# Kernel tuning notes

Hardware: AMD Instinct MI355X
Metric: run time of the kernel (lower is better)

Reference implementation:

```python
import jax, jax.numpy as jnp
import numpy as np

H = 10   # GRU hidden size
L = 10   # num layers
E = 400  # embedding dim
V = 100000
T, B = 84, 96


def gru_layer(x, w_ih, w_hh, b_ih, b_hh, reverse):
    # x: (T, B, in_dim); w_ih: (3H, in_dim); w_hh: (3H, H)
    xp = jnp.einsum('tbi,gi->tbg', x, w_ih) + b_ih  # (T, B, 3H)
    if reverse:
        xp = xp[::-1]

    def step(h, xt):
        gh = h @ w_hh.T + b_hh
        xr, xz, xn = jnp.split(xt, 3, axis=-1)
        hr, hz, hn = jnp.split(gh, 3, axis=-1)
        r = jax.nn.sigmoid(xr + hr)
        z = jax.nn.sigmoid(xz + hz)
        n = jnp.tanh(xn + r * hn)
        h_new = (1.0 - z) * n + z * h
        return h_new, h_new

    h0 = jnp.zeros((x.shape[1], H), x.dtype)
    _, ys = jax.lax.scan(step, h0, xp)
    if reverse:
        ys = ys[::-1]
    return ys  # (T, B, H)


def setup_inputs():
    key = jax.random.key(0)
    ks = jax.random.split(key, 12)
    s = 0.05
    return {
        'x': jax.random.randint(ks[0], (T, B), 0, V),
        'emb': jax.random.normal(ks[1], (V, E), jnp.float32) * 0.1,
        'w_ih0': jax.random.normal(ks[2], (2, 3 * H, E), jnp.float32) * s,
        'w_hh0': jax.random.normal(ks[3], (2, 3 * H, H), jnp.float32) * s,
        'b_ih0': jax.random.normal(ks[4], (2, 3 * H), jnp.float32) * s,
        'b_hh0': jax.random.normal(ks[5], (2, 3 * H), jnp.float32) * s,
        'w_ih': jax.random.normal(ks[6], (L - 1, 2, 3 * H, 2 * H), jnp.float32) * s,
        'w_hh': jax.random.normal(ks[7], (L - 1, 2, 3 * H, H), jnp.float32) * s,
        'b_ih': jax.random.normal(ks[8], (L - 1, 2, 3 * H), jnp.float32) * s,
        'b_hh': jax.random.normal(ks[9], (L - 1, 2, 3 * H), jnp.float32) * s,
        'lin_w': jax.random.normal(ks[10], (19, 336), jnp.float32) * s,
        'lin_b': jax.random.normal(ks[11], (19,), jnp.float32) * s,
    }


def reference(x, emb, w_ih0, w_hh0, b_ih0, b_hh0, w_ih, w_hh, b_ih, b_hh, lin_w, lin_b):
    out = emb[x]  # (T, B, 400)
    for l in range(L):
        if l == 0:
            wi, wh, bi, bh = w_ih0, w_hh0, b_ih0, b_hh0
        else:
            wi, wh, bi, bh = w_ih[l - 1], w_hh[l - 1], b_ih[l - 1], b_hh[l - 1]
        fwd = gru_layer(out, wi[0], wh[0], bi[0], bh[0], False)
        bwd = gru_layer(out, wi[1], wh[1], bi[1], bh[1], True)
        out = jnp.concatenate([fwd, bwd], axis=-1)  # (T, B, 20)
        # dropout p=0.2 between layers is disabled (eval-mode reference)
    # AvgPool2d(3)/MaxPool2d(3) on 3D input pool over (batch, feature) dims
    trimmed = out[:, : (B // 3) * 3, :18].reshape(T, B // 3, 3, 6, 3)
    avg = trimmed.mean(axis=(2, 4))  # (T, B//3, 6)
    mx = trimmed.max(axis=(2, 4))    # (T, B//3, 6)
    cat = jnp.concatenate([avg, mx], axis=2)  # (T, B//3, 12)
    flat = cat.reshape(-1, 336)  # (96, 336)
    # dropout p=0.2 disabled (eval-mode reference)
    return jax.nn.sigmoid(flat @ lin_w.T + lin_b)
```

## Files before the change

kernel.cpp:

```cpp
#include <hip/hip_runtime.h>
#include <math.h>

#define TT 84
#define BB 96
#define GB 6
#define NG 16
#define NTOK (TT*BB)
#define RW4 6

#define S_RZ (-1.4426950408889634f)
#define S_N  (-2.8853900817779268f)

__device__ __forceinline__ float frcp(float x)  { return __builtin_amdgcn_rcpf(x); }
__device__ __forceinline__ float fexp2(float x) { return __builtin_amdgcn_exp2f(x); }

__global__ __launch_bounds__(256) void proj0_kernel(
    const int* __restrict__ x, const float* __restrict__ emb,
    const float* __restrict__ wih0, const float* __restrict__ bih0,
    float* __restrict__ xp, unsigned int* __restrict__ bar)
{
    if (blockIdx.x == 0 && threadIdx.x == 0) bar[0] = 0u;
    __shared__ float4 xrow[32][100];
    const int tok0 = blockIdx.x * 32;
    for (int u = threadIdx.x; u < 32*100; u += 256) {
        int tk = u / 100, i4 = u % 100;
        int row = x[tok0 + tk];
        xrow[tk][i4] = ((const float4*)emb)[row*100 + i4];
    }
    __syncthreads();
    const int g64 = threadIdx.x & 63;
    const int q   = threadIdx.x >> 6;
    if (g64 >= 60) return;
    const int dir = g64 / 30, gg = g64 % 30;
    const float sc = (gg < 20) ? S_RZ : S_N;
    const float bias = bih0[dir*30 + gg];
    float acc[8];
    #pragma unroll
    for (int c = 0; c < 8; ++c) acc[c] = bias;
    const float4* w4 = ((const float4*)wih0) + (dir*30 + gg)*100;
    for (int i4 = 0; i4 < 100; ++i4) {
        float4 w = w4[i4];
        #pragma unroll
        for (int c = 0; c < 8; ++c) {
            float4 xv = xrow[q*8 + c][i4];
            acc[c] += w.x*xv.x + w.y*xv.y + w.z*xv.z + w.w*xv.w;
        }
    }
    #pragma unroll
    for (int c = 0; c < 8; ++c) {
        int tok = tok0 + q*8 + c;
        int t = tok / BB, b = tok % BB;
        xp[((size_t)((dir*TT + t)*BB + b))*30 + gg] = acc[c]*sc;
    }
}

__device__ __forceinline__ float gru_cell(
    float xr, float xz, float xn,
    float4 ha, float4 hb, float4 hc,
    const float* wr, const float* wz, const float* wn,
    float bhr, float bhz, float bhn, float& hown)
{
    float hr0 = fmaf(wr[0], ha.x, bhr), hr1 = wr[1]*ha.y;
    float hz0 = fmaf(wz[0], ha.x, bhz), hz1 = wz[1]*ha.y;
    float hn0 = fmaf(wn[0], ha.x, bhn), hn1 = wn[1]*ha.y;
    hr0 = fmaf(wr[2], ha.z, hr0); hr1 = fmaf(wr[3], ha.w, hr1);
    hz0 = fmaf(wz[2], ha.z, hz0); hz1 = fmaf(wz[3], ha.w, hz1);
    hn0 = fmaf(wn[2], ha.z, hn0); hn1 = fmaf(wn[3], ha.w, hn1);
    hr0 = fmaf(wr[4], hb.x, hr0); hr1 = fmaf(wr[5], hb.y, hr1);
    hz0 = fmaf(wz[4], hb.x, hz0); hz1 = fmaf(wz[5], hb.y, hz1);
    hn0 = fmaf(wn[4], hb.x, hn0); hn1 = fmaf(wn[5], hb.y, hn1);
    hr0 = fmaf(wr[6], hb.z, hr0); hr1 = fmaf(wr[7], hb.w, hr1);
    hz0 = fmaf(wz[6], hb.z, hz0); hz1 = fmaf(wz[7], hb.w, hz1);
    hn0 = fmaf(wn[6], hb.z, hn0); hn1 = fmaf(wn[7], hb.w, hn1);
    hr0 = fmaf(wr[8], hc.x, hr0); hr1 = fmaf(wr[9], hc.y, hr1);
    hz0 = fmaf(wz[8], hc.x, hz0); hz1 = fmaf(wz[9], hc.y, hz1);
    hn0 = fmaf(wn[8], hc.x, hn0); hn1 = fmaf(wn[9], hc.y, hn1);
    float r = frcp(1.f + fexp2(xr + hr0 + hr1));
    float z = frcp(1.f + fexp2(xz + hz0 + hz1));
    float an = fmaf(r, hn0 + hn1, xn);
    float n  = fmaf(2.f, frcp(1.f + fexp2(an)), -1.f);
    float hnew = n + z*(hown - n);
    hown = hnew;
    return hnew;
}

__device__ __forceinline__ void proj20(
    const float4* A, const float* wpr, const float* wpz, const float* wpn,
    float bir, float biz, float bin, float& xr, float& xz, float& xn)
{
    float a[24];
    #pragma unroll
    for (int q = 0; q < 6; ++q) {
        a[4*q]=A[q].x; a[4*q+1]=A[q].y; a[4*q+2]=A[q].z; a[4*q+3]=A[q].w;
    }
    xr = bir; xz = biz; xn = bin;
    #pragma unroll
    for (int c = 0; c < 20; ++c) {
        float av = a[c + (c >= 10 ? 2 : 0)];
        xr = fmaf(wpr[c], av, xr); xz = fmaf(wpz[c], av, xz); xn = fmaf(wpn[c], av, xn);
    }
}

template<bool LAST>
__device__ __forceinline__ void gru_mid(
    const float* __restrict__ wi, const float* __restrict__ bi,
    const float* __restrict__ wh, const float* __restrict__ bh,
    const float4* in4, float4* out4, float* __restrict__ actG,
    int bl, int j, bool act_ln, int b, int dir, int dt, int t0)
{
    float wpr[20], wpz[20], wpn[20];
    {
        const float4* p0 = (const float4*)(wi + j*20);
        const float4* p1 = (const float4*)(wi + (10+j)*20);
        const float4* p2 = (const float4*)(wi + (20+j)*20);
        #pragma unroll
        for (int q = 0; q < 5; ++q) {
            float4 a = p0[q]; wpr[4*q]=a.x*S_RZ; wpr[4*q+1]=a.y*S_RZ; wpr[4*q+2]=a.z*S_RZ; wpr[4*q+3]=a.w*S_RZ;
            float4 c = p1[q]; wpz[4*q]=c.x*S_RZ; wpz[4*q+1]=c.y*S_RZ; wpz[4*q+2]=c.z*S_RZ; wpz[4*q+3]=c.w*S_RZ;
            float4 d = p2[q]; wpn[4*q]=d.x*S_N;  wpn[4*q+1]=d.y*S_N;  wpn[4*q+2]=d.z*S_N;  wpn[4*q+3]=d.w*S_N;
        }
    }
    const float bir = bi[j]*S_RZ, biz = bi[10+j]*S_RZ, bin = bi[20+j]*S_N;
    float wr[10], wz[10], wn[10];
    {
        const float2* p0 = (const float2*)(wh + j*10);
        const float2* p1 = (const float2*)(wh + (10+j)*10);
        const float2* p2 = (const float2*)(wh + (20+j)*10);
        #pragma unroll
        for (int q = 0; q < 5; ++q) {
            float2 a = p0[q]; wr[2*q]=a.x*S_RZ; wr[2*q+1]=a.y*S_RZ;
            float2 c = p1[q]; wz[2*q]=c.x*S_RZ; wz[2*q+1]=c.y*S_RZ;
            float2 d = p2[q]; wn[2*q]=d.x*S_N;  wn[2*q+1]=d.y*S_N;
        }
    }
    const float bhr = bh[j]*S_RZ, bhz = bh[10+j]*S_RZ, bhn = bh[20+j]*S_N;

    float4 ha = {0,0,0,0}, hb = {0,0,0,0}, hc = {0,0,0,0};
    float hown = 0.f;
    float4 A[6], B[6];
    float xr_c, xz_c, xn_c, xr_n, xz_n, xn_n;
    int t = t0;
    {
        const float4* p0 = &in4[(t0*GB + bl)*RW4];
        #pragma unroll
        for (int q = 0; q < 6; ++q) B[q] = p0[q];
        const float4* p1 = &in4[((t0 + dt)*GB + bl)*RW4];
        #pragma unroll
        for (int q = 0; q < 6; ++q) A[q] = p1[q];
        proj20(B, wpr, wpz, wpn, bir, biz, bin, xr_c, xz_c, xn_c);
    }

    #pragma unroll 1
    for (int s = 0; s < TT; s += 2) {
        {
            float hnew = gru_cell(xr_c, xz_c, xn_c, ha, hb, hc, wr, wz, wn, bhr, bhz, bhn, hown);
            ((float*)&out4[(t*GB + bl)*RW4])[dir*12 + j] = hnew;
            const float4* hr = &out4[(t*GB + bl)*RW4 + dir*3];
            ha = hr[0]; hb = hr[1]; hc = hr[2];
            __builtin_amdgcn_sched_barrier(0);
            if (LAST && act_ln) actG[(size_t)(t*BB + b)*20 + dir*10 + j] = hnew;
            int tl = t + 2*dt; tl = tl < 0 ? 0 : (tl > TT-1 ? TT-1 : tl);
            const float4* pl = &in4[(tl*GB + bl)*RW4];
            #pragma unroll
            for (int q = 0; q < 6; ++q) B[q] = pl[q];
            proj20(A, wpr, wpz, wpn, bir, biz, bin, xr_n, xz_n, xn_n);
            t += dt;
        }
        {
            float hnew = gru_cell(xr_n, xz_n, xn_n, ha, hb, hc, wr, wz, wn, bhr, bhz, bhn, hown);
            ((float*)&out4[(t*GB + bl)*RW4])[dir*12 + j] = hnew;
            const float4* hr = &out4[(t*GB + bl)*RW4 + dir*3];
            ha = hr[0]; hb = hr[1]; hc = hr[2];
            __builtin_amdgcn_sched_barrier(0);
            if (LAST && act_ln) actG[(size_t)(t*BB + b)*20 + dir*10 + j] = hnew;
            int tl = t + 2*dt; tl = tl < 0 ? 0 : (tl > TT-1 ? TT-1 : tl);
            const float4* pl = &in4[(tl*GB + bl)*RW4];
            #pragma unroll
            for (int q = 0; q < 6; ++q) A[q] = pl[q];
            proj20(B, wpr, wpz, wpn, bir, biz, bin, xr_c, xz_c, xn_c);
            t += dt;
        }
    }
}

__global__ __launch_bounds__(128, 1) void mega_kernel(
    const float* __restrict__ xp0,
    const float* __restrict__ whh0, const float* __restrict__ bhh0,
    const float* __restrict__ wih,  const float* __restrict__ bih,
    const float* __restrict__ whh,  const float* __restrict__ bhh,
    const float* __restrict__ lin_w, const float* __restrict__ lin_b,
    float* __restrict__ actG, unsigned int* __restrict__ bar,
    float* __restrict__ out)
{
    __shared__ float4 actA4[TT*GB*RW4];
    __shared__ float4 actB4[TT*GB*RW4];

    const int tid  = threadIdx.x;
    const int dir  = tid >> 6;
    const int lane = tid & 63;
    int bl = lane / 10; if (bl > 5) bl = 5;
    int j  = lane - bl*10; if (j > 9) j = 9;
    const bool act_ln = (lane < 60);
    const int grp = blockIdx.x;
    const int b   = grp*GB + bl;
    const int dt  = dir ? -1 : 1;
    const int t0  = dir ? TT-1 : 0;

    {
        float wr[10], wz[10], wn[10];
        const float* wh = whh0 + dir*300;
        {
            const float2* p0 = (const float2*)(wh + j*10);
            const float2* p1 = (const float2*)(wh + (10+j)*10);
            const float2* p2 = (const float2*)(wh + (20+j)*10);
            #pragma unroll
            for (int q = 0; q < 5; ++q) {
                float2 a = p0[q]; wr[2*q]=a.x*S_RZ; wr[2*q+1]=a.y*S_RZ;
                float2 c = p1[q]; wz[2*q]=c.x*S_RZ; wz[2*q+1]=c.y*S_RZ;
                float2 d = p2[q]; wn[2*q]=d.x*S_N;  wn[2*q+1]=d.y*S_N;
            }
        }
        const float bhr = bhh0[dir*30 + j]*S_RZ;
        const float bhz = bhh0[dir*30 + 10 + j]*S_RZ;
        const float bhn = bhh0[dir*30 + 20 + j]*S_N;

        float4 ha = {0,0,0,0}, hb = {0,0,0,0}, hc = {0,0,0,0};
        float hown = 0.f;
        int t = t0;
        const float* xb = xp0 + (size_t)dir*TT*BB*30;

        float xr_c = xb[(size_t)(t*BB + b)*30 + j];
        float xz_c = xb[(size_t)(t*BB + b)*30 + 10 + j];
        float xn_c = xb[(size_t)(t*BB + b)*30 + 20 + j];

        #pragma unroll 1
        for (int s = 0; s < TT; ++s) {
            float hnew = gru_cell(xr_c, xz_c, xn_c, ha, hb, hc, wr, wz, wn, bhr, bhz, bhn, hown);
            ((float*)&actA4[(t*GB + bl)*RW4])[dir*12 + j] = hnew;
            const float4* hr = &actA4[(t*GB + bl)*RW4 + dir*3];
            ha = hr[0]; hb = hr[1]; hc = hr[2];
            __builtin_amdgcn_sched_barrier(0);
            int tn = (s == TT-1) ? t : t + dt;
            xr_c = xb[(size_t)(tn*BB + b)*30 + j];
            xz_c = xb[(size_t)(tn*BB + b)*30 + 10 + j];
            xn_c = xb[(size_t)(tn*BB + b)*30 + 20 + j];
            t = tn;
        }
    }
    __syncthreads();

    #pragma unroll 1
    for (int lp = 0; lp < 4; ++lp) {
        int l = 1 + lp*2;
        gru_mid<false>(wih + (size_t)((l-1)*2 + dir)*600, bih + (size_t)((l-1)*2 + dir)*30,
                       whh + (size_t)((l-1)*2 + dir)*300, bhh + (size_t)((l-1)*2 + dir)*30,
                       actA4, actB4, actG, bl, j, act_ln, b, dir, dt, t0);
        __syncthreads();
        l = 2 + lp*2;
        gru_mid<false>(wih + (size_t)((l-1)*2 + dir)*600, bih + (size_t)((l-1)*2 + dir)*30,
                       whh + (size_t)((l-1)*2 + dir)*300, bhh + (size_t)((l-1)*2 + dir)*30,
                       actB4, actA4, actG, bl, j, act_ln, b, dir, dt, t0);
        __syncthreads();
    }
    gru_mid<true>(wih + (size_t)(8*2 + dir)*600, bih + (size_t)(8*2 + dir)*30,
                  whh + (size_t)(8*2 + dir)*300, bhh + (size_t)(8*2 + dir)*30,
                  actA4, actB4, actG, bl, j, act_ln, b, dir, dt, t0);

    __threadfence();
    __syncthreads();
    if (tid == 0) {
        __hip_atomic_fetch_add(bar, 1u, __ATOMIC_ACQ_REL, __HIP_MEMORY_SCOPE_AGENT);
        while (__hip_atomic_load(bar, __ATOMIC_ACQUIRE, __HIP_MEMORY_SCOPE_AGENT) < (unsigned)NG)
            __builtin_amdgcn_s_sleep(1);
    }
    __syncthreads();
    __threadfence();

    float* feat = (float*)actA4;
    for (int u = tid; u < GB*336; u += 128) {
        int q = u / 336, v = u % 336;
        int r = grp*GB + q;
        int qq = v / 12, f = v % 12;
        int pair = r*28 + qq;
        int t = pair / 32, bb = pair % 32;
        int jj = (f < 6) ? f : f - 6;
        float acc = (f < 6) ? 0.f : -1e30f;
        #pragma unroll
        for (int i = 0; i < 3; ++i) {
            #pragma unroll
            for (int kk = 0; kk < 3; ++kk) {
                float vv = actG[(size_t)(t*BB + bb*3 + i)*20 + jj*3 + kk];
                if (f < 6) acc += vv; else acc = fmaxf(acc, vv);
            }
        }
        feat[u] = (f < 6) ? acc*(1.f/9.f) : acc;
    }
    __syncthreads();
    if (tid < GB*19) {
        int q = tid / 19, o = tid % 19;
        int r = grp*GB + q;
        float acc = lin_b[o];
        const float* wrow = lin_w + o*336;
        const float* frow = feat + q*336;
        for (int v = 0; v < 336; ++v) acc = fmaf(frow[v], wrow[v], acc);
        out[r*19 + o] = frcp(1.f + __expf(-acc));
    }
}

extern "C" void kernel_launch(void* const* d_in, const int* in_sizes, int n_in,
                              void* d_out, int out_size, void* d_ws, size_t ws_size,
                              hipStream_t stream)
{
    const int*   x     = (const int*)  d_in[0];
    const float* emb   = (const float*)d_in[1];
    const float* wih0  = (const float*)d_in[2];
    const float* whh0  = (const float*)d_in[3];
    const float* bih0  = (const float*)d_in[4];
    const float* bhh0  = (const float*)d_in[5];
    const float* wih   = (const float*)d_in[6];
    const float* whh   = (const float*)d_in[7];
    const float* bih   = (const float*)d_in[8];
    const float* bhh   = (const float*)d_in[9];
    const float* lin_w = (const float*)d_in[10];
    const float* lin_b = (const float*)d_in[11];
    float* out = (float*)d_out;

    float* xp0  = (float*)d_ws;
    float* actG = xp0 + (size_t)2*NTOK*30;
    unsigned int* bar = (unsigned int*)(actG + (size_t)NTOK*20);

    proj0_kernel<<<252, 256, 0, stream>>>(x, emb, wih0, bih0, xp0, bar);
    mega_kernel<<<NG, 128, 0, stream>>>(xp0, whh0, bhh0, wih, bih, whh, bhh,
                                        lin_w, lin_b, actG, bar, out);
}
```

Measured before the change: 485.9 us.

## Split GRU layers into producer projection waves and consumer recurrence waves

Each block now runs 256 threads. Two waves compute the input projection for a layer and publish each timestep into shared memory, signalling progress through per-layer flags. The other two waves run the serial recurrence and spin on those flags, so the 20-wide projection leaves the recurrent critical path. Inter-layer activations move from shared memory to global buffers, and the hidden-state exchange uses a small shared buffer. The cost is flag polling, global-memory activation traffic, and the second activation buffer aliasing the layer-0 projection workspace, which other blocks may still be reading.

```diff
diff --git a/kernel.cpp b/kernel.cpp
--- a/kernel.cpp
+++ b/kernel.cpp
@@ -5,8 +5,9 @@
 #define BB 96
 #define GB 6
 #define NG 16
+#define NL 10
 #define NTOK (TT*BB)
-#define RW4 6
+#define XPS 37
 
 #define S_RZ (-1.4426950408889634f)
 #define S_N  (-2.8853900817779268f)
@@ -56,7 +57,7 @@
 
 __device__ __forceinline__ float gru_cell(
     float xr, float xz, float xn,
-    float4 ha, float4 hb, float4 hc,
+    float4 ha, float4 hb, float2 hc,
     const float* wr, const float* wz, const float* wn,
     float bhr, float bhz, float bhn, float& hown)
 {
@@ -84,187 +85,168 @@
     return hnew;
 }
 
-__device__ __forceinline__ void proj20(
-    const float4* A, const float* wpr, const float* wpz, const float* wpn,
-    float bir, float biz, float bin, float& xr, float& xz, float& xn)
-{
-    float a[24];
-    #pragma unroll
-    for (int q = 0; q < 6; ++q) {
-        a[4*q]=A[q].x; a[4*q+1]=A[q].y; a[4*q+2]=A[q].z; a[4*q+3]=A[q].w;
-    }
-    xr = bir; xz = biz; xn = bin;
-    #pragma unroll
-    for (int c = 0; c < 20; ++c) {
-        float av = a[c + (c >= 10 ? 2 : 0)];
-        xr = fmaf(wpr[c], av, xr); xz = fmaf(wpz[c], av, xz); xn = fmaf(wpn[c], av, xn);
-    }
-}
-
-template<bool LAST>
-__device__ __forceinline__ void gru_mid(
-    const float* __restrict__ wi, const float* __restrict__ bi,
-    const float* __restrict__ wh, const float* __restrict__ bh,
-    const float4* in4, float4* out4, float* __restrict__ actG,
-    int bl, int j, bool act_ln, int b, int dir, int dt, int t0)
-{
-    float wpr[20], wpz[20], wpn[20];
-    {
-        const float4* p0 = (const float4*)(wi + j*20);
-        const float4* p1 = (const float4*)(wi + (10+j)*20);
-        const float4* p2 = (const float4*)(wi + (20+j)*20);
-        #pragma unroll
-        for (int q = 0; q < 5; ++q) {
-            float4 a = p0[q]; wpr[4*q]=a.x*S_RZ; wpr[4*q+1]=a.y*S_RZ; wpr[4*q+2]=a.z*S_RZ; wpr[4*q+3]=a.w*S_RZ;
-            float4 c = p1[q]; wpz[4*q]=c.x*S_RZ; wpz[4*q+1]=c.y*S_RZ; wpz[4*q+2]=c.z*S_RZ; wpz[4*q+3]=c.w*S_RZ;
-            float4 d = p2[q]; wpn[4*q]=d.x*S_N;  wpn[4*q+1]=d.y*S_N;  wpn[4*q+2]=d.z*S_N;  wpn[4*q+3]=d.w*S_N;
-        }
-    }
-    const float bir = bi[j]*S_RZ, biz = bi[10+j]*S_RZ, bin = bi[20+j]*S_N;
-    float wr[10], wz[10], wn[10];
-    {
-        const float2* p0 = (const float2*)(wh + j*10);
-        const float2* p1 = (const float2*)(wh + (10+j)*10);
-        const float2* p2 = (const float2*)(wh + (20+j)*10);
-        #pragma unroll
-        for (int q = 0; q < 5; ++q) {
-            float2 a = p0[q]; wr[2*q]=a.x*S_RZ; wr[2*q+1]=a.y*S_RZ;
-            float2 c = p1[q]; wz[2*q]=c.x*S_RZ; wz[2*q+1]=c.y*S_RZ;
-            float2 d = p2[q]; wn[2*q]=d.x*S_N;  wn[2*q+1]=d.y*S_N;
-        }
-    }
-    const float bhr = bh[j]*S_RZ, bhz = bh[10+j]*S_RZ, bhn = bh[20+j]*S_N;
-
-    float4 ha = {0,0,0,0}, hb = {0,0,0,0}, hc = {0,0,0,0};
-    float hown = 0.f;
-    float4 A[6], B[6];
-    float xr_c, xz_c, xn_c, xr_n, xz_n, xn_n;
-    int t = t0;
-    {
-        const float4* p0 = &in4[(t0*GB + bl)*RW4];
-        #pragma unroll
-        for (int q = 0; q < 6; ++q) B[q] = p0[q];
-        const float4* p1 = &in4[((t0 + dt)*GB + bl)*RW4];
-        #pragma unroll
-        for (int q = 0; q < 6; ++q) A[q] = p1[q];
-        proj20(B, wpr, wpz, wpn, bir, biz, bin, xr_c, xz_c, xn_c);
-    }
-
-    #pragma unroll 1
-    for (int s = 0; s < TT; s += 2) {
-        {
-            float hnew = gru_cell(xr_c, xz_c, xn_c, ha, hb, hc, wr, wz, wn, bhr, bhz, bhn, hown);
-            ((float*)&out4[(t*GB + bl)*RW4])[dir*12 + j] = hnew;
-            const float4* hr = &out4[(t*GB + bl)*RW4 + dir*3];
-            ha = hr[0]; hb = hr[1]; hc = hr[2];
-            __builtin_amdgcn_sched_barrier(0);
-            if (LAST && act_ln) actG[(size_t)(t*BB + b)*20 + dir*10 + j] = hnew;
-            int tl = t + 2*dt; tl = tl < 0 ? 0 : (tl > TT-1 ? TT-1 : tl);
-            const float4* pl = &in4[(tl*GB + bl)*RW4];
-            #pragma unroll
-            for (int q = 0; q < 6; ++q) B[q] = pl[q];
-            proj20(A, wpr, wpz, wpn, bir, biz, bin, xr_n, xz_n, xn_n);
-            t += dt;
-        }
-        {
-            float hnew = gru_cell(xr_n, xz_n, xn_n, ha, hb, hc, wr, wz, wn, bhr, bhz, bhn, hown);
-            ((float*)&out4[(t*GB + bl)*RW4])[dir*12 + j] = hnew;
-            const float4* hr = &out4[(t*GB + bl)*RW4 + dir*3];
-            ha = hr[0]; hb = hr[1]; hc = hr[2];
-            __builtin_amdgcn_sched_barrier(0);
-            if (LAST && act_ln) actG[(size_t)(t*BB + b)*20 + dir*10 + j] = hnew;
-            int tl = t + 2*dt; tl = tl < 0 ? 0 : (tl > TT-1 ? TT-1 : tl);
-            const float4* pl = &in4[(tl*GB + bl)*RW4];
-            #pragma unroll
-            for (int q = 0; q < 6; ++q) A[q] = pl[q];
-            proj20(B, wpr, wpz, wpn, bir, biz, bin, xr_c, xz_c, xn_c);
-            t += dt;
-        }
-    }
-}
-
-__global__ __launch_bounds__(128, 1) void mega_kernel(
+__device__ __forceinline__ void waitflag(int* f, int needed)
+{
+    int fv = __hip_atomic_load(f, __ATOMIC_ACQUIRE, __HIP_MEMORY_SCOPE_WORKGROUP);
+    while (fv < needed)
+        fv = __hip_atomic_load(f, __ATOMIC_ACQUIRE, __HIP_MEMORY_SCOPE_WORKGROUP);
+}
+
+__global__ __launch_bounds__(256, 1) void mega_kernel(
     const float* __restrict__ xp0,
     const float* __restrict__ whh0, const float* __restrict__ bhh0,
     const float* __restrict__ wih,  const float* __restrict__ bih,
     const float* __restrict__ whh,  const float* __restrict__ bhh,
     const float* __restrict__ lin_w, const float* __restrict__ lin_b,
-    float* __restrict__ actG, unsigned int* __restrict__ bar,
-    float* __restrict__ out)
-{
-    __shared__ float4 actA4[TT*GB*RW4];
-    __shared__ float4 actB4[TT*GB*RW4];
+    float* __restrict__ actA, float* __restrict__ actB,
+    unsigned int* __restrict__ bar, float* __restrict__ out)
+{
+    __shared__ float xpS[2*TT*GB*XPS];
+    __shared__ float hbuf[2][GB][12];
+    __shared__ int   flagsS[NL][2];
 
     const int tid  = threadIdx.x;
-    const int dir  = tid >> 6;
+    const int wave = tid >> 6;
     const int lane = tid & 63;
     int bl = lane / 10; if (bl > 5) bl = 5;
     int j  = lane - bl*10; if (j > 9) j = 9;
     const bool act_ln = (lane < 60);
     const int grp = blockIdx.x;
     const int b   = grp*GB + bl;
+
+    if (tid < NL*2) ((int*)flagsS)[tid] = 0;
+    __syncthreads();
+
+    const int dir = wave & 1;
     const int dt  = dir ? -1 : 1;
     const int t0  = dir ? TT-1 : 0;
 
-    {
-        float wr[10], wz[10], wn[10];
-        const float* wh = whh0 + dir*300;
-        {
-            const float2* p0 = (const float2*)(wh + j*10);
-            const float2* p1 = (const float2*)(wh + (10+j)*10);
-            const float2* p2 = (const float2*)(wh + (20+j)*10);
-            #pragma unroll
-            for (int q = 0; q < 5; ++q) {
-                float2 a = p0[q]; wr[2*q]=a.x*S_RZ; wr[2*q+1]=a.y*S_RZ;
-                float2 c = p1[q]; wz[2*q]=c.x*S_RZ; wz[2*q+1]=c.y*S_RZ;
-                float2 d = p2[q]; wn[2*q]=d.x*S_N;  wn[2*q+1]=d.y*S_N;
+    #pragma unroll 1
+    for (int l = 0; l < NL; ++l) {
+        if (wave < 2) {
+            const float* whL = (l==0) ? (whh0 + dir*300) : (whh + (size_t)((l-1)*2+dir)*300);
+            const float* bhL = (l==0) ? (bhh0 + dir*30)  : (bhh + (size_t)((l-1)*2+dir)*30);
+            float* actW = (l & 1) ? actB : actA;
+            int* flag = &flagsS[l][dir];
+
+            float wr[10], wz[10], wn[10];
+            {
+                const float2* p0 = (const float2*)(whL + j*10);
+                const float2* p1 = (const float2*)(whL + (10+j)*10);
+                const float2* p2 = (const float2*)(whL + (20+j)*10);
+                #pragma unroll
+                for (int q = 0; q < 5; ++q) {
+                    float2 a = p0[q]; wr[2*q]=a.x*S_RZ; wr[2*q+1]=a.y*S_RZ;
+                    float2 c = p1[q]; wz[2*q]=c.x*S_RZ; wz[2*q+1]=c.y*S_RZ;
+                    float2 d = p2[q]; wn[2*q]=d.x*S_N;  wn[2*q+1]=d.y*S_N;
+                }
+            }
+            const float bhr = bhL[j]*S_RZ, bhz = bhL[10+j]*S_RZ, bhn = bhL[20+j]*S_N;
+
+            float4 ha = {0,0,0,0}, hb4 = {0,0,0,0};
+            float2 hc2 = {0,0};
+            float hown = 0.f;
+
+            waitflag(flag, 1);
+            int base0 = ((dir*TT + t0)*GB + bl)*XPS;
+            float xc0 = xpS[base0+j], xc1 = xpS[base0+10+j], xc2 = xpS[base0+20+j];
+            waitflag(flag, 2);
+            int base1 = ((dir*TT + (t0+dt))*GB + bl)*XPS;
+            float xn0 = xpS[base1+j], xn1 = xpS[base1+10+j], xn2 = xpS[base1+20+j];
+
+            const float4* hp = (const float4*)&hbuf[dir][bl][0];
+            int t = t0;
+            #pragma unroll 2
+            for (int s = 0; s < TT; ++s) {
+                float hnew = gru_cell(xc0,xc1,xc2, ha,hb4,hc2, wr,wz,wn, bhr,bhz,bhn, hown);
+                hbuf[dir][bl][j] = hnew;
+                ha  = hp[0];
+                hb4 = hp[1];
+                hc2 = ((const float2*)hp)[4];
+                __builtin_amdgcn_sched_barrier(0);
+                if (act_ln) actW[(size_t)(t*BB + b)*20 + dir*10 + j] = hnew;
+                int sp = s + 2;
+                int needed = (sp+1 > TT) ? TT : sp+1;
+                waitflag(flag, needed);
+                int tp = t0 + dt*sp; tp = tp < 0 ? 0 : (tp > TT-1 ? TT-1 : tp);
+                int bp = ((dir*TT + tp)*GB + bl)*XPS;
+                float p0 = xpS[bp+j], p1 = xpS[bp+10+j], p2 = xpS[bp+20+j];
+                xc0 = xn0; xc1 = xn1; xc2 = xn2;
+                xn0 = p0;  xn1 = p1;  xn2 = p2;
+                t += dt;
+            }
+        } else {
+            int* flag = &flagsS[l][dir];
+            if (l == 0) {
+                const float* xg = xp0 + (size_t)dir*TT*BB*30;
+                int t = t0;
+                int g0 = (t*BB + b)*30;
+                float a0 = xg[g0+j], a1 = xg[g0+10+j], a2 = xg[g0+20+j];
+                #pragma unroll 1
+                for (int srow = 0; srow < TT; ++srow) {
+                    int tn = (srow == TT-1) ? t : t + dt;
+                    int gn = (tn*BB + b)*30;
+                    float n0 = xg[gn+j], n1 = xg[gn+10+j], n2 = xg[gn+20+j];
+                    int bo = ((dir*TT + t)*GB + bl)*XPS;
+                    xpS[bo+j] = a0; xpS[bo+10+j] = a1; xpS[bo+20+j] = a2;
+                    if (lane == 0)
+                        __hip_atomic_store(flag, srow+1, __ATOMIC_RELEASE, __HIP_MEMORY_SCOPE_WORKGROUP);
+                    a0 = n0; a1 = n1; a2 = n2; t = tn;
+                }
+            } else {
+                const float* wiL = wih + (size_t)((l-1)*2 + dir)*600;
+                const float* biL = bih + (size_t)((l-1)*2 + dir)*30;
+                float wpr[20], wpz[20], wpn[20];
+                {
+                    const float4* p0 = (const float4*)(wiL + j*20);
+                    const float4* p1 = (const float4*)(wiL + (10+j)*20);
+                    const float4* p2 = (const float4*)(wiL + (20+j)*20);
+                    #pragma unroll
+                    for (int q = 0; q < 5; ++q) {
+                        float4 a = p0[q]; wpr[4*q]=a.x*S_RZ; wpr[4*q+1]=a.y*S_RZ; wpr[4*q+2]=a.z*S_RZ; wpr[4*q+3]=a.w*S_RZ;
+                        float4 c = p1[q]; wpz[4*q]=c.x*S_RZ; wpz[4*q+1]=c.y*S_RZ; wpz[4*q+2]=c.z*S_RZ; wpz[4*q+3]=c.w*S_RZ;
+                        float4 d = p2[q]; wpn[4*q]=d.x*S_N;  wpn[4*q+1]=d.y*S_N;  wpn[4*q+2]=d.z*S_N;  wpn[4*q+3]=d.w*S_N;
+                    }
+                }
+                const float bir = biL[j]*S_RZ, biz = biL[10+j]*S_RZ, bin = biL[20+j]*S_N;
+                const float* actR = (l & 1) ? actA : actB;
+                float4 A[5], Bv[5];
+                int t = t0;
+                {
+                    const float4* ap = (const float4*)(actR + (size_t)(t*BB + b)*20);
+                    #pragma unroll
+                    for (int q = 0; q < 5; ++q) A[q] = ap[q];
+                }
+                #pragma unroll 1
+                for (int srow = 0; srow < TT; ++srow) {
+                    int tn = (srow == TT-1) ? t : t + dt;
+                    const float4* ap = (const float4*)(actR + (size_t)(tn*BB + b)*20);
+                    #pragma unroll
+                    for (int q = 0; q < 5; ++q) Bv[q] = ap[q];
+                    float av[20];
+                    #pragma unroll
+                    for (int q = 0; q < 5; ++q) {
+                        av[4*q]=A[q].x; av[4*q+1]=A[q].y; av[4*q+2]=A[q].z; av[4*q+3]=A[q].w;
+                    }
+                    float xr = bir, xz = biz, xn = bin;
+                    #pragma unroll
+                    for (int c = 0; c < 20; ++c) {
+                        xr = fmaf(wpr[c], av[c], xr);
+                        xz = fmaf(wpz[c], av[c], xz);
+                        xn = fmaf(wpn[c], av[c], xn);
+                    }
+                    int bo = ((dir*TT + t)*GB + bl)*XPS;
+                    xpS[bo+j] = xr; xpS[bo+10+j] = xz; xpS[bo+20+j] = xn;
+                    if (lane == 0)
+                        __hip_atomic_store(flag, srow+1, __ATOMIC_RELEASE, __HIP_MEMORY_SCOPE_WORKGROUP);
+                    #pragma unroll
+                    for (int q = 0; q < 5; ++q) A[q] = Bv[q];
+                    t = tn;
+                }
             }
         }
-        const float bhr = bhh0[dir*30 + j]*S_RZ;
-        const float bhz = bhh0[dir*30 + 10 + j]*S_RZ;
-        const float bhn = bhh0[dir*30 + 20 + j]*S_N;
-
-        float4 ha = {0,0,0,0}, hb = {0,0,0,0}, hc = {0,0,0,0};
-        float hown = 0.f;
-        int t = t0;
-        const float* xb = xp0 + (size_t)dir*TT*BB*30;
-
-        float xr_c = xb[(size_t)(t*BB + b)*30 + j];
-        float xz_c = xb[(size_t)(t*BB + b)*30 + 10 + j];
-        float xn_c = xb[(size_t)(t*BB + b)*30 + 20 + j];
-
-        #pragma unroll 1
-        for (int s = 0; s < TT; ++s) {
-            float hnew = gru_cell(xr_c, xz_c, xn_c, ha, hb, hc, wr, wz, wn, bhr, bhz, bhn, hown);
-            ((float*)&actA4[(t*GB + bl)*RW4])[dir*12 + j] = hnew;
-            const float4* hr = &actA4[(t*GB + bl)*RW4 + dir*3];
-            ha = hr[0]; hb = hr[1]; hc = hr[2];
-            __builtin_amdgcn_sched_barrier(0);
-            int tn = (s == TT-1) ? t : t + dt;
-            xr_c = xb[(size_t)(tn*BB + b)*30 + j];
-            xz_c = xb[(size_t)(tn*BB + b)*30 + 10 + j];
-            xn_c = xb[(size_t)(tn*BB + b)*30 + 20 + j];
-            t = tn;
-        }
-    }
-    __syncthreads();
-
-    #pragma unroll 1
-    for (int lp = 0; lp < 4; ++lp) {
-        int l = 1 + lp*2;
-        gru_mid<false>(wih + (size_t)((l-1)*2 + dir)*600, bih + (size_t)((l-1)*2 + dir)*30,
-                       whh + (size_t)((l-1)*2 + dir)*300, bhh + (size_t)((l-1)*2 + dir)*30,
-                       actA4, actB4, actG, bl, j, act_ln, b, dir, dt, t0);
         __syncthreads();
-        l = 2 + lp*2;
-        gru_mid<false>(wih + (size_t)((l-1)*2 + dir)*600, bih + (size_t)((l-1)*2 + dir)*30,
-                       whh + (size_t)((l-1)*2 + dir)*300, bhh + (size_t)((l-1)*2 + dir)*30,
-                       actB4, actA4, actG, bl, j, act_ln, b, dir, dt, t0);
-        __syncthreads();
-    }
-    gru_mid<true>(wih + (size_t)(8*2 + dir)*600, bih + (size_t)(8*2 + dir)*30,
-                  whh + (size_t)(8*2 + dir)*300, bhh + (size_t)(8*2 + dir)*30,
-                  actA4, actB4, actG, bl, j, act_ln, b, dir, dt, t0);
+    }
 
     __threadfence();
     __syncthreads();
@@ -276,8 +258,8 @@
     __syncthreads();
     __threadfence();
 
-    float* feat = (float*)actA4;
-    for (int u = tid; u < GB*336; u += 128) {
+    float* feat = xpS;
+    for (int u = tid; u < GB*336; u += 256) {
         int q = u / 336, v = u % 336;
         int r = grp*GB + q;
         int qq = v / 12, f = v % 12;
@@ -289,7 +271,7 @@
         for (int i = 0; i < 3; ++i) {
             #pragma unroll
             for (int kk = 0; kk < 3; ++kk) {
-                float vv = actG[(size_t)(t*BB + bb*3 + i)*20 + jj*3 + kk];
+                float vv = actB[(size_t)(t*BB + bb*3 + i)*20 + jj*3 + kk];
                 if (f < 6) acc += vv; else acc = fmaxf(acc, vv);
             }
         }
@@ -326,10 +308,11 @@
     float* out = (float*)d_out;
 
     float* xp0  = (float*)d_ws;
-    float* actG = xp0 + (size_t)2*NTOK*30;
-    unsigned int* bar = (unsigned int*)(actG + (size_t)NTOK*20);
+    float* actA = xp0 + (size_t)2*NTOK*30;
+    unsigned int* bar = (unsigned int*)(actA + (size_t)NTOK*20);
+    float* actB = xp0;
 
     proj0_kernel<<<252, 256, 0, stream>>>(x, emb, wih0, bih0, xp0, bar);
-    mega_kernel<<<NG, 128, 0, stream>>>(xp0, whh0, bhh0, wih, bih, whh, bhh,
-                                        lin_w, lin_b, actG, bar, out);
-}
+    mega_kernel<<<NG, 256, 0, stream>>>(xp0, whh0, bhh0, wih, bih, whh, bhh,
+                                        lin_w, lin_b, actA, actB, bar, out);
+}
```

Result: no change. 492.0 us (+1.3%).
